# Optimization experiments

Measured on AMD Instinct MI355X. Metric: run time of the kernel, lower is better.

## Reference

```python
import jax, jax.numpy as jnp
import numpy as np

N, KLEN, Q, S, E, H = 8, 512, 16, 128, 256, 8


def setup_inputs() -> dict:
    key = jax.random.key(0)
    ks = jax.random.split(key, 9)
    values = jax.random.normal(ks[0], (N, KLEN, E), dtype=jnp.float32)
    keys = jax.random.normal(ks[1], (N, KLEN, E), dtype=jnp.float32)
    query = jax.random.normal(ks[2], (N, Q, S, E), dtype=jnp.float32)
    mask = jax.random.randint(ks[3], (N, 1, 1, KLEN, 1), 0, 2, dtype=jnp.int32)
    Wv = jax.random.normal(ks[4], (E, E), dtype=jnp.float32) * 0.02
    Wk = jax.random.normal(ks[5], (E, E), dtype=jnp.float32) * 0.02
    Wq = jax.random.normal(ks[6], (E, E), dtype=jnp.float32) * 0.02
    Wo = jax.random.normal(ks[7], (E, H * E), dtype=jnp.float32) * 0.02
    bo = jnp.zeros((E,), dtype=jnp.float32)
    return {"values": values, "keys": keys, "query": query, "mask": mask,
            "Wv": Wv, "Wk": Wk, "Wq": Wq, "Wo": Wo, "bo": bo}


def reference(values, keys, query, mask, Wv, Wk, Wq, Wo, bo):
    # In the torch module head_dim == embed_size and the SAME Linear is applied
    # to every (expanded) head, so project once and broadcast over heads.
    e = Wq.shape[0]
    heads = Wo.shape[1] // e
    v = values @ Wv.T          # [N, K, E]
    k = keys @ Wk.T            # [N, K, E]
    q = query @ Wq.T           # [N, Q, S, E]
    # energy per head is identical; broadcast to [N, H, Q, K, S] to mirror
    # torch's einsum('nqshd,nkhd->nhqks') followed by masked_fill.
    energy = jnp.einsum('nqsd,nkd->nqks', q, k)               # [N, Q, K, S]
    energy = jnp.broadcast_to(energy[:, None],
                              (energy.shape[0], heads) + energy.shape[1:])
    energy = jnp.where(mask == 0, jnp.float32(-1e20), energy)  # [N,H,Q,K,S]
    attn = jax.nn.softmax(energy / jnp.sqrt(jnp.float32(e)), axis=3)
    out = jnp.einsum('nhqks,nkd->nqshd', attn, v)              # [N,Q,S,H,E]
    out = out.reshape(out.shape[0], out.shape[1], out.shape[2], heads * e)
    return out @ Wo.T + bo                                     # [N, Q, S, E]
```

## Files before the change

kernel.cpp:

```cpp
#include <hip/hip_runtime.h>
#include <hip/hip_bf16.h>
#include <stdint.h>

#define NB   8
#define KL   512
#define QD   16
#define SD   128
#define ED   256
#define RPN  (QD*SD)
#define BMR  64
#define FRAG 512
#define PAN  131072

typedef __hip_bfloat16 bf16;
using s16x8 = __attribute__((ext_vector_type(8))) short;
using f32x4 = __attribute__((ext_vector_type(4))) float;

__device__ __forceinline__ float b2f(unsigned short u){
    union { uint32_t i; float f; } v; v.i = ((uint32_t)u) << 16; return v.f;
}
__device__ __forceinline__ float b2f_hi(uint32_t u){
    union { uint32_t i; float f; } v; v.i = u & 0xFFFF0000u; return v.f;
}
__device__ __forceinline__ float b2f_lo(uint32_t u){
    union { uint32_t i; float f; } v; v.i = u << 16; return v.f;
}
__device__ __forceinline__ unsigned short f2b(float f){
    union { float ff; uint32_t i; } v; v.ff = f;
    uint32_t lsb = (v.i >> 16) & 1;
    v.i += 0x7FFFu + lsb;
    return (unsigned short)(v.i >> 16);
}
__device__ __forceinline__ uint32_t cvtpk(float lo, float hi){
    uint32_t r;
    asm("v_cvt_pk_bf16_f32 %0, %1, %2" : "=v"(r) : "v"(lo), "v"(hi));
    return r;
}
__device__ __forceinline__ f32x4 mfma16(s16x8 a, s16x8 b, f32x4 c){
    return __builtin_amdgcn_mfma_f32_16x16x32_bf16(a, b, c, 0, 0, 0);
}

template<bool B>
__device__ __forceinline__ float ldin(const void* p, size_t i){
    if (B) return b2f(((const unsigned short*)p)[i]);
    else   return ((const float*)p)[i];
}

__device__ bool probe_bf16(const uint32_t* __restrict__ w, int* pc){
    if (threadIdx.x == 0) *pc = 0;
    __syncthreads();
    if (threadIdx.x < 256){
        int local = 0;
        #pragma unroll
        for (int i = 0; i < 4; ++i){
            uint32_t x = w[threadIdx.x*4 + i];
            uint32_t e = (x >> 7) & 0xFFu;
            local += (e >= 120u && e <= 132u) ? 1 : 0;
        }
        if (local) atomicAdd(pc, local);
    }
    __syncthreads();
    return *pc > 512;
}

__device__ __forceinline__ int waddr(int i, int o){
    return (((o >> 4)*8 + (i >> 5)) << 9) + (((o & 15) | (((i >> 3) & 3) << 4)) << 3) + (i & 7);
}

template<bool B>
__device__ void gt_body(const void* __restrict__ Wq, const void* __restrict__ Wk,
                        unsigned short* __restrict__ WgH,
                        unsigned short* __restrict__ WgL, int bx){
    int b = bx, a = threadIdx.x;
    float s = 0.f;
    #pragma unroll 8
    for (int d = 0; d < 256; ++d)
        s += ldin<B>(Wq, (size_t)d*256 + a) * ldin<B>(Wk, (size_t)d*256 + b);
    unsigned short hi = f2b(s);
    unsigned short lo = f2b(s - b2f(hi));
    int ad = waddr(b, a);
    WgH[ad] = hi; WgL[ad] = lo;
}
template<bool B>
__device__ void wosmt_body(const void* __restrict__ Wo, const void* __restrict__ Wv,
                           unsigned short* __restrict__ WmH,
                           unsigned short* __restrict__ WmL, int bx, float (*sm)[256]){
    int t = threadIdx.x, e0 = bx*8;
    #pragma unroll
    for (int je = 0; je < 8; ++je){
        int e = e0 + je;
        float s = 0.f;
        #pragma unroll
        for (int h = 0; h < 8; ++h) s += ldin<B>(Wo, (size_t)e*2048 + h*256 + t);
        sm[je][t] = s;
    }
    __syncthreads();
    float acc[8] = {0,0,0,0,0,0,0,0};
    #pragma unroll 4
    for (int dp = 0; dp < 256; ++dp){
        float wv = ldin<B>(Wv, (size_t)dp*256 + t);
        #pragma unroll
        for (int je = 0; je < 8; ++je) acc[je] += sm[je][dp] * wv;
    }
    #pragma unroll
    for (int je = 0; je < 8; ++je){
        unsigned short hi = f2b(acc[je]);
        unsigned short lo = f2b(acc[je] - b2f(hi));
        int ad = waddr(t, e0 + je);
        WmH[ad] = hi; WmL[ad] = lo;
    }
}
__global__ __launch_bounds__(256)
void k_prep(const void* __restrict__ values,
            const void* __restrict__ Wq, const void* __restrict__ Wk,
            const void* __restrict__ Wo, const void* __restrict__ Wv,
            unsigned short* __restrict__ WgH, unsigned short* __restrict__ WgL,
            unsigned short* __restrict__ WmH, unsigned short* __restrict__ WmL){
    __shared__ float sm[8][256];
    __shared__ int pc;
    bool bf = probe_bf16((const uint32_t*)values, &pc);
    if (blockIdx.x < 256){
        if (bf) gt_body<true >(Wq, Wk, WgH, WgL, blockIdx.x);
        else    gt_body<false>(Wq, Wk, WgH, WgL, blockIdx.x);
    } else {
        int bx = blockIdx.x - 256;
        if (bf) wosmt_body<true >(Wo, Wv, WmH, WmL, bx, sm);
        else    wosmt_body<false>(Wo, Wv, WmH, WmL, bx, sm);
    }
}

template<bool B>
__device__ void projM_body(const void* __restrict__ A,
                           const unsigned short* __restrict__ WH,
                           const unsigned short* __restrict__ WL,
                           unsigned short* __restrict__ outF,
                           int bx, bool keysHalf, unsigned short* St){
    int t = threadIdx.x, lane = t & 63, w = t >> 6;
    int l15 = t & 15, g = (t >> 4) & 3;
    int n   = bx >> 4;
    int r0n = (bx & 15) * 32;
    int r0  = n*512 + r0n;

    f32x4 acc[2][2];
    #pragma unroll
    for (int rt = 0; rt < 2; ++rt)
        #pragma unroll
        for (int c = 0; c < 2; ++c) acc[rt][c] = (f32x4){0.f,0.f,0.f,0.f};

    s16x8 wh[3][2], wl[3][2];
    auto LDW = [&](int ks, int sl){
        #pragma unroll
        for (int c = 0; c < 2; ++c){
            size_t off = (size_t)(((w*2 + c)*8 + ks)*512 + lane*8);
            wh[sl][c] = *(const s16x8*)(WH + off);
            wl[sl][c] = *(const s16x8*)(WL + off);
        }
    };
    float4 ar[2][2][2];
    s16x8  ab[2][2];
    auto LDA = [&](int ks, int sl){
        #pragma unroll
        for (int rt = 0; rt < 2; ++rt){
            size_t idx = (size_t)(r0 + rt*16 + l15)*256 + ks*32 + g*8;
            if (B) ab[sl][rt] = *(const s16x8*)((const unsigned short*)A + idx);
            else { ar[sl][rt][0] = *(const float4*)((const float*)A + idx);
                   ar[sl][rt][1] = *(const float4*)((const float*)A + idx + 4); }
        }
    };
    LDW(0,0); LDW(1,1); LDA(0,0); LDA(1,1);

    #pragma unroll
    for (int ks = 0; ks < 8; ++ks){
        int s = ks & 1, sw = ks % 3;
        s16x8 ah[2], al[2];
        #pragma unroll
        for (int rt = 0; rt < 2; ++rt){
            if (B){
                ah[rt] = ab[s][rt];
            } else {
                union { s16x8 v; uint32_t u[4]; } H, L;
                float4 x0 = ar[s][rt][0], x1 = ar[s][rt][1];
                H.u[0] = cvtpk(x0.x, x0.y); H.u[1] = cvtpk(x0.z, x0.w);
                H.u[2] = cvtpk(x1.x, x1.y); H.u[3] = cvtpk(x1.z, x1.w);
                L.u[0] = cvtpk(x0.x - b2f_lo(H.u[0]), x0.y - b2f_hi(H.u[0]));
                L.u[1] = cvtpk(x0.z - b2f_lo(H.u[1]), x0.w - b2f_hi(H.u[1]));
                L.u[2] = cvtpk(x1.x - b2f_lo(H.u[2]), x1.y - b2f_hi(H.u[2]));
                L.u[3] = cvtpk(x1.z - b2f_lo(H.u[3]), x1.w - b2f_hi(H.u[3]));
                ah[rt] = H.v; al[rt] = L.v;
            }
        }
        if (ks + 2 < 8) LDA(ks + 2, s);
        #pragma unroll
        for (int rt = 0; rt < 2; ++rt)
            #pragma unroll
            for (int c = 0; c < 2; ++c){
                acc[rt][c] = mfma16(ah[rt], wh[sw][c], acc[rt][c]);
                if (!B) acc[rt][c] = mfma16(al[rt], wh[sw][c], acc[rt][c]);
                acc[rt][c] = mfma16(ah[rt], wl[sw][c], acc[rt][c]);
            }
        if (ks + 2 < 8) LDW(ks + 2, (ks + 2) % 3);
    }

    #pragma unroll
    for (int rt = 0; rt < 2; ++rt){
        #pragma unroll
        for (int c = 0; c < 2; ++c){
            #pragma unroll
            for (int j = 0; j < 4; ++j){
                int rloc = g*4 + j;
                int col  = (w*2 + c)*16 + l15;
                int idx;
                if (keysHalf)
                    idx = rt*4096 + ((col >> 5) << 9)
                        + ((rloc | (((col >> 3) & 3) << 4)) << 3) + (col & 7);
                else {
                    int kl = rt*16 + rloc;
                    idx = ((col >> 4) << 9)
                        + (((col & 15) | ((kl >> 3) << 4)) << 3) + (kl & 7);
                }
                St[idx] = f2b(acc[rt][c][j]);
            }
        }
    }
    __syncthreads();

    #pragma unroll
    for (int h = 0; h < 2; ++h){
        int s8 = t*8 + h*4096;
        if (keysHalf){
            size_t base = (size_t)n*PAN + (size_t)((r0n >> 4)*8)*512;
            *(s16x8*)(outF + base + s8) = *(const s16x8*)(St + s8);
        } else {
            int ks2 = r0n >> 5;
            int fl = s8 >> 9, off = s8 & 511;
            *(s16x8*)(outF + (size_t)n*PAN + (size_t)((fl*16 + ks2)*512 + off))
                = *(const s16x8*)(St + s8);
        }
    }
}
__global__ __launch_bounds__(512)
void k_projM(const void* __restrict__ keys, const void* __restrict__ values,
             const unsigned short* __restrict__ WgH, const unsigned short* __restrict__ WgL,
             const unsigned short* __restrict__ WmH, const unsigned short* __restrict__ WmL,
             unsigned short* __restrict__ kkF, unsigned short* __restrict__ utF){
    __shared__ unsigned short St[8192];
    __shared__ int pc;
    bool bf = probe_bf16((const uint32_t*)values, &pc);
    int bx = blockIdx.x;
    bool keysHalf = (bx < 128);
    int bxl = bx & 127;
    if (keysHalf){
        if (bf) projM_body<true >(keys, WgH, WgL, kkF, bxl, true, St);
        else    projM_body<false>(keys, WgH, WgL, kkF, bxl, true, St);
    } else {
        if (bf) projM_body<true >(values, WmH, WmL, utF, bxl, false, St);
        else    projM_body<false>(values, WmH, WmL, utF, bxl, false, St);
    }
}

template<bool B>
__device__ void fused_body(const void* __restrict__ query,
                           const unsigned short* __restrict__ kkF,
                           const unsigned short* __restrict__ utF,
                           const int* __restrict__ mask,
                           const void* __restrict__ bo,
                           void* __restrict__ out,
                           unsigned short* Qs, unsigned short* Pf,
                           float* redM, float* redS){
    int bid = blockIdx.x;
    int n   = bid & 7;
    int r0  = (bid >> 3) * BMR;
    int t   = threadIdx.x;
    int l15 = t & 15;
    int g   = (t >> 4) & 3;
    int w   = t >> 6;
    int lane = t & 63;

    const unsigned short* Kn = kkF + (size_t)n*PAN;
    const unsigned short* Un = utF + (size_t)n*PAN;
    const int* mn = mask + n*KL;

    #pragma unroll
    for (int rr = 0; rr < 2; ++rr){
        int row = rr*32 + (t >> 4);
        int c0  = (t & 15) * 16;
        int sw  = (row & 7) << 3;
        size_t qoff = (size_t)n*RPN*ED + (size_t)(r0 + row)*ED + c0;
        if (B){
            const unsigned short* qp = (const unsigned short*)query + qoff;
            s16x8 v0 = *(const s16x8*)(qp);
            s16x8 v1 = *(const s16x8*)(qp + 8);
            *(s16x8*)&Qs[(row*ED + c0    ) ^ sw] = v0;
            *(s16x8*)&Qs[(row*ED + c0 + 8) ^ sw] = v1;
        } else {
            const float* qp = (const float*)query + qoff;
            float4 x0 = *(const float4*)(qp);
            float4 x1 = *(const float4*)(qp + 4);
            float4 x2 = *(const float4*)(qp + 8);
            float4 x3 = *(const float4*)(qp + 12);
            union { s16x8 v; uint32_t u[4]; } pk;
            pk.u[0] = cvtpk(x0.x,x0.y); pk.u[1] = cvtpk(x0.z,x0.w);
            pk.u[2] = cvtpk(x1.x,x1.y); pk.u[3] = cvtpk(x1.z,x1.w);
            *(s16x8*)&Qs[(row*ED + c0    ) ^ sw] = pk.v;
            pk.u[0] = cvtpk(x2.x,x2.y); pk.u[1] = cvtpk(x2.z,x2.w);
            pk.u[2] = cvtpk(x3.x,x3.y); pk.u[3] = cvtpk(x3.z,x3.w);
            *(s16x8*)&Qs[(row*ED + c0 + 8) ^ sw] = pk.v;
        }
    }
    __syncthreads();

    int asw = (l15 & 7) << 3;

    f32x4 acc1[4][4];
    {
        #pragma unroll
        for (int rt = 0; rt < 4; ++rt)
            #pragma unroll
            for (int c = 0; c < 4; ++c) acc1[rt][c] = (f32x4){0.f,0.f,0.f,0.f};

        const unsigned short* kb = Kn + (size_t)w*16384 + (size_t)lane*8;
        s16x8 bb[3][4];
        auto LDK = [&](int KS, int SL){
            #pragma unroll
            for (int c = 0; c < 4; ++c)
                bb[SL][c] = *(const s16x8*)(kb + (size_t)(c*8 + KS)*FRAG);
        };
        LDK(0,0); LDK(1,1);
        #pragma unroll
        for (int ks = 0; ks < 8; ++ks){
            if (ks + 2 < 8) LDK(ks + 2, (ks + 2) % 3);
            int col = ks*32 + g*8;
            #pragma unroll
            for (int rt = 0; rt < 4; ++rt){
                s16x8 a = *(const s16x8*)&Qs[((rt*16 + l15)*ED + col) ^ asw];
                #pragma unroll
                for (int c = 0; c < 4; ++c)
                    acc1[rt][c] = mfma16(a, bb[ks % 3][c], acc1[rt][c]);
            }
        }
        #pragma unroll
        for (int c = 0; c < 4; ++c){
            bool zz = (mn[w*64 + c*16 + l15] == 0);
            #pragma unroll
            for (int rt = 0; rt < 4; ++rt)
                #pragma unroll
                for (int j = 0; j < 4; ++j)
                    acc1[rt][c][j] = zz ? -1e20f : acc1[rt][c][j] * 0.0625f;
        }
    }

    {
        #pragma unroll
        for (int rt = 0; rt < 4; ++rt)
            #pragma unroll
            for (int j = 0; j < 4; ++j){
                float m0 = fmaxf(fmaxf(acc1[rt][0][j], acc1[rt][1][j]),
                                 fmaxf(acc1[rt][2][j], acc1[rt][3][j]));
                #pragma unroll
                for (int off = 1; off < 16; off <<= 1)
                    m0 = fmaxf(m0, __shfl_xor(m0, off, 16));
                if (l15 == 0) redM[(rt*16 + g*4 + j)*8 + w] = m0;
            }
        __syncthreads();
        #pragma unroll
        for (int rt = 0; rt < 4; ++rt)
            #pragma unroll
            for (int j = 0; j < 4; ++j){
                int row = rt*16 + g*4 + j;
                float4 a = *(const float4*)&redM[row*8];
                float4 b = *(const float4*)&redM[row*8 + 4];
                float m = fmaxf(fmaxf(fmaxf(a.x,a.y),fmaxf(a.z,a.w)),
                                fmaxf(fmaxf(b.x,b.y),fmaxf(b.z,b.w)));
                float s = 0.f;
                #pragma unroll
                for (int c = 0; c < 4; ++c){
                    acc1[rt][c][j] = __expf(acc1[rt][c][j] - m);
                    s += acc1[rt][c][j];
                }
                #pragma unroll
                for (int off = 1; off < 16; off <<= 1)
                    s += __shfl_xor(s, off, 16);
                if (l15 == 0) redS[row*8 + w] = s;
            }
        __syncthreads();
        int ihi = ((l15 >> 3) << 4);
        int ilo = l15 & 7;
        #pragma unroll
        for (int rt = 0; rt < 4; ++rt){
            #pragma unroll
            for (int j = 0; j < 4; ++j){
                int row = rt*16 + g*4 + j;
                float4 a = *(const float4*)&redS[row*8];
                float4 b = *(const float4*)&redS[row*8 + 4];
                float inv = 1.0f / ((a.x+a.y+a.z+a.w) + (b.x+b.y+b.z+b.w));
                #pragma unroll
                for (int c = 0; c < 4; ++c){
                    int lp = (g*4 + j) | (((c & 1) << 5) | ihi);
                    int elem = (rt*16 + w*2 + (c >> 1))*FRAG + lp*8 + ilo;
                    Pf[elem] = f2b(acc1[rt][c][j] * inv);
                }
            }
        }
    }
    __syncthreads();

    {
        f32x4 acc2[4][2];
        #pragma unroll
        for (int rt = 0; rt < 4; ++rt)
            #pragma unroll
            for (int c = 0; c < 2; ++c) acc2[rt][c] = (f32x4){0.f,0.f,0.f,0.f};

        const unsigned short* ub = Un + (size_t)(2*w)*8192 + (size_t)lane*8;
        s16x8 bu[3][2];
        auto LDU = [&](int KS, int SL){
            #pragma unroll
            for (int c = 0; c < 2; ++c)
                bu[SL][c] = *(const s16x8*)(ub + (size_t)(c*16 + KS)*FRAG);
        };
        LDU(0,0); LDU(1,1);
        #pragma unroll
        for (int ks = 0; ks < 16; ++ks){
            if (ks + 2 < 16) LDU(ks + 2, (ks + 2) % 3);
            #pragma unroll
            for (int rt = 0; rt < 4; ++rt){
                s16x8 p = *(const s16x8*)&Pf[(rt*16 + ks)*FRAG + lane*8];
                #pragma unroll
                for (int c = 0; c < 2; ++c)
                    acc2[rt][c] = mfma16(p, bu[ks % 3][c], acc2[rt][c]);
            }
        }
        float bov[2];
        #pragma unroll
        for (int c = 0; c < 2; ++c) bov[c] = ldin<B>(bo, (2*w + c)*16 + l15);
        #pragma unroll
        for (int rt = 0; rt < 4; ++rt){
            #pragma unroll
            for (int j = 0; j < 4; ++j){
                int row = rt*16 + g*4 + j;
                #pragma unroll
                for (int c = 0; c < 2; ++c){
                    int e = (2*w + c)*16 + l15;
                    float val = acc2[rt][c][j] + bov[c];
                    size_t oidx = (size_t)n*RPN*ED + (size_t)(r0 + row)*ED + e;
                    if (B) ((unsigned short*)out)[oidx] = f2b(val);
                    else   ((float*)out)[oidx] = val;
                }
            }
        }
    }
}

__global__ __launch_bounds__(512, 2)
void k_fused5(const void* __restrict__ values, const void* __restrict__ query,
              const unsigned short* __restrict__ kkF,
              const unsigned short* __restrict__ utF,
              const int* __restrict__ mask, const void* __restrict__ bo,
              void* __restrict__ out){
    __shared__ unsigned short Qs[BMR*ED];
    __shared__ unsigned short Pf[64*FRAG];
    __shared__ float redM[BMR*8];
    __shared__ float redS[BMR*8];
    __shared__ int pc;
    bool bf = probe_bf16((const uint32_t*)values, &pc);
    if (bf) fused_body<true >(query, kkF, utF, mask, bo, out, Qs, Pf, redM, redS);
    else    fused_body<false>(query, kkF, utF, mask, bo, out, Qs, Pf, redM, redS);
}

extern "C" void kernel_launch(void* const* d_in, const int* in_sizes, int n_in,
                              void* d_out, int out_size, void* d_ws, size_t ws_size,
                              hipStream_t stream){
    const void* values = d_in[0];
    const void* keys   = d_in[1];
    const void* query  = d_in[2];
    const int*  mask   = (const int*)d_in[3];
    const void* Wv     = d_in[4];
    const void* Wk     = d_in[5];
    const void* Wq     = d_in[6];
    const void* Wo     = d_in[7];
    const void* bo     = d_in[8];

    unsigned short* wsu = (unsigned short*)d_ws;
    unsigned short* wgh = wsu;
    unsigned short* wgl = wsu + 65536;
    unsigned short* wmh = wsu + 131072;
    unsigned short* wml = wsu + 196608;
    unsigned short* ws_kk = wsu + 262144;
    unsigned short* ws_u  = ws_kk + (size_t)NB*PAN;

    k_prep  <<< 288, 256, 0, stream>>>(values, Wq, Wk, Wo, Wv, wgh, wgl, wmh, wml);
    k_projM <<< 256, 512, 0, stream>>>(keys, values, wgh, wgl, wmh, wml, ws_kk, ws_u);
    k_fused5<<< 256, 512, 0, stream>>>(values, query, ws_kk, ws_u, mask, bo, d_out);
}
```

Before: 144.8 us.

## Halve fused attention row tile and split prep reductions across 512 threads

```diff
diff --git a/kernel.cpp b/kernel.cpp
--- a/kernel.cpp
+++ b/kernel.cpp
@@ -8,7 +8,7 @@
 #define SD   128
 #define ED   256
 #define RPN  (QD*SD)
-#define BMR  64
+#define BMR  32
 #define FRAG 512
 #define PAN  131072
 
@@ -70,62 +70,81 @@
 template<bool B>
 __device__ void gt_body(const void* __restrict__ Wq, const void* __restrict__ Wk,
                         unsigned short* __restrict__ WgH,
-                        unsigned short* __restrict__ WgL, int bx){
-    int b = bx, a = threadIdx.x;
+                        unsigned short* __restrict__ WgL, int bx,
+                        float (*ps)[2048]){
+    int t = threadIdx.x;
+    int a = t & 255, hf = t >> 8;
+    int b = bx;
+    int d0 = hf * 128;
     float s = 0.f;
     #pragma unroll 8
-    for (int d = 0; d < 256; ++d)
+    for (int d = d0; d < d0 + 128; ++d)
         s += ldin<B>(Wq, (size_t)d*256 + a) * ldin<B>(Wk, (size_t)d*256 + b);
-    unsigned short hi = f2b(s);
-    unsigned short lo = f2b(s - b2f(hi));
-    int ad = waddr(b, a);
-    WgH[ad] = hi; WgL[ad] = lo;
+    ps[hf][a] = s;
+    __syncthreads();
+    if (t < 256){
+        float v = ps[0][t] + ps[1][t];
+        unsigned short hi = f2b(v);
+        unsigned short lo = f2b(v - b2f(hi));
+        int ad = waddr(b, t);
+        WgH[ad] = hi; WgL[ad] = lo;
+    }
 }
 template<bool B>
 __device__ void wosmt_body(const void* __restrict__ Wo, const void* __restrict__ Wv,
                            unsigned short* __restrict__ WmH,
-                           unsigned short* __restrict__ WmL, int bx, float (*sm)[256]){
-    int t = threadIdx.x, e0 = bx*8;
+                           unsigned short* __restrict__ WmL, int bx,
+                           float (*sm)[256], float (*ps)[2048]){
+    int t = threadIdx.x, d = t & 255, hf = t >> 8, e0 = bx*8;
     #pragma unroll
-    for (int je = 0; je < 8; ++je){
-        int e = e0 + je;
+    for (int jj = 0; jj < 4; ++jj){
+        int je = hf*4 + jj;
+        int e  = e0 + je;
         float s = 0.f;
         #pragma unroll
-        for (int h = 0; h < 8; ++h) s += ldin<B>(Wo, (size_t)e*2048 + h*256 + t);
-        sm[je][t] = s;
+        for (int h = 0; h < 8; ++h) s += ldin<B>(Wo, (size_t)e*2048 + h*256 + d);
+        sm[je][d] = s;
     }
     __syncthreads();
     float acc[8] = {0,0,0,0,0,0,0,0};
+    int dp0 = hf * 128;
     #pragma unroll 4
-    for (int dp = 0; dp < 256; ++dp){
-        float wv = ldin<B>(Wv, (size_t)dp*256 + t);
+    for (int dp = dp0; dp < dp0 + 128; ++dp){
+        float wv = ldin<B>(Wv, (size_t)dp*256 + d);
         #pragma unroll
         for (int je = 0; je < 8; ++je) acc[je] += sm[je][dp] * wv;
     }
     #pragma unroll
-    for (int je = 0; je < 8; ++je){
-        unsigned short hi = f2b(acc[je]);
-        unsigned short lo = f2b(acc[je] - b2f(hi));
-        int ad = waddr(t, e0 + je);
-        WmH[ad] = hi; WmL[ad] = lo;
-    }
-}
-__global__ __launch_bounds__(256)
+    for (int je = 0; je < 8; ++je) ps[hf][d*8 + je] = acc[je];
+    __syncthreads();
+    if (t < 256){
+        #pragma unroll
+        for (int je = 0; je < 8; ++je){
+            float v = ps[0][t*8 + je] + ps[1][t*8 + je];
+            unsigned short hi = f2b(v);
+            unsigned short lo = f2b(v - b2f(hi));
+            int ad = waddr(t, e0 + je);
+            WmH[ad] = hi; WmL[ad] = lo;
+        }
+    }
+}
+__global__ __launch_bounds__(512)
 void k_prep(const void* __restrict__ values,
             const void* __restrict__ Wq, const void* __restrict__ Wk,
             const void* __restrict__ Wo, const void* __restrict__ Wv,
             unsigned short* __restrict__ WgH, unsigned short* __restrict__ WgL,
             unsigned short* __restrict__ WmH, unsigned short* __restrict__ WmL){
     __shared__ float sm[8][256];
+    __shared__ float ps[2][2048];
     __shared__ int pc;
     bool bf = probe_bf16((const uint32_t*)values, &pc);
     if (blockIdx.x < 256){
-        if (bf) gt_body<true >(Wq, Wk, WgH, WgL, blockIdx.x);
-        else    gt_body<false>(Wq, Wk, WgH, WgL, blockIdx.x);
+        if (bf) gt_body<true >(Wq, Wk, WgH, WgL, blockIdx.x, ps);
+        else    gt_body<false>(Wq, Wk, WgH, WgL, blockIdx.x, ps);
     } else {
         int bx = blockIdx.x - 256;
-        if (bf) wosmt_body<true >(Wo, Wv, WmH, WmL, bx, sm);
-        else    wosmt_body<false>(Wo, Wv, WmH, WmL, bx, sm);
+        if (bf) wosmt_body<true >(Wo, Wv, WmH, WmL, bx, sm, ps);
+        else    wosmt_body<false>(Wo, Wv, WmH, WmL, bx, sm, ps);
     }
 }
 
@@ -280,9 +299,8 @@
     const unsigned short* Un = utF + (size_t)n*PAN;
     const int* mn = mask + n*KL;
 
-    #pragma unroll
-    for (int rr = 0; rr < 2; ++rr){
-        int row = rr*32 + (t >> 4);
+    {
+        int row = t >> 4;
         int c0  = (t & 15) * 16;
         int sw  = (row & 7) << 3;
         size_t qoff = (size_t)n*RPN*ED + (size_t)(r0 + row)*ED + c0;
@@ -311,10 +329,11 @@
 
     int asw = (l15 & 7) << 3;
 
-    f32x4 acc1[4][4];
+    float p[2][4][4];
     {
-        #pragma unroll
-        for (int rt = 0; rt < 4; ++rt)
+        f32x4 acc1[2][4];
+        #pragma unroll
+        for (int rt = 0; rt < 2; ++rt)
             #pragma unroll
             for (int c = 0; c < 4; ++c) acc1[rt][c] = (f32x4){0.f,0.f,0.f,0.f};
 
@@ -330,40 +349,49 @@
         for (int ks = 0; ks < 8; ++ks){
             if (ks + 2 < 8) LDK(ks + 2, (ks + 2) % 3);
             int col = ks*32 + g*8;
-            #pragma unroll
-            for (int rt = 0; rt < 4; ++rt){
-                s16x8 a = *(const s16x8*)&Qs[((rt*16 + l15)*ED + col) ^ asw];
-                #pragma unroll
-                for (int c = 0; c < 4; ++c)
-                    acc1[rt][c] = mfma16(a, bb[ks % 3][c], acc1[rt][c]);
+            s16x8 a0 = *(const s16x8*)&Qs[(( 0 + l15)*ED + col) ^ asw];
+            s16x8 a1 = *(const s16x8*)&Qs[((16 + l15)*ED + col) ^ asw];
+            #pragma unroll
+            for (int c = 0; c < 4; ++c){
+                acc1[0][c] = mfma16(a0, bb[ks % 3][c], acc1[0][c]);
+                acc1[1][c] = mfma16(a1, bb[ks % 3][c], acc1[1][c]);
             }
         }
         #pragma unroll
         for (int c = 0; c < 4; ++c){
             bool zz = (mn[w*64 + c*16 + l15] == 0);
             #pragma unroll
-            for (int rt = 0; rt < 4; ++rt)
+            for (int rt = 0; rt < 2; ++rt)
                 #pragma unroll
                 for (int j = 0; j < 4; ++j)
-                    acc1[rt][c][j] = zz ? -1e20f : acc1[rt][c][j] * 0.0625f;
+                    p[rt][c][j] = zz ? -1e20f : acc1[rt][c][j] * 0.0625f;
         }
     }
 
     {
-        #pragma unroll
-        for (int rt = 0; rt < 4; ++rt)
+        float mx[2][4];
+        #pragma unroll
+        for (int rt = 0; rt < 2; ++rt)
             #pragma unroll
             for (int j = 0; j < 4; ++j){
-                float m0 = fmaxf(fmaxf(acc1[rt][0][j], acc1[rt][1][j]),
-                                 fmaxf(acc1[rt][2][j], acc1[rt][3][j]));
+                float m0 = fmaxf(fmaxf(p[rt][0][j], p[rt][1][j]),
+                                 fmaxf(p[rt][2][j], p[rt][3][j]));
                 #pragma unroll
                 for (int off = 1; off < 16; off <<= 1)
                     m0 = fmaxf(m0, __shfl_xor(m0, off, 16));
-                if (l15 == 0) redM[(rt*16 + g*4 + j)*8 + w] = m0;
-            }
+                mx[rt][j] = m0;
+            }
+        if (l15 == 0){
+            #pragma unroll
+            for (int rt = 0; rt < 2; ++rt)
+                #pragma unroll
+                for (int j = 0; j < 4; ++j)
+                    redM[(rt*16 + g*4 + j)*8 + w] = mx[rt][j];
+        }
         __syncthreads();
-        #pragma unroll
-        for (int rt = 0; rt < 4; ++rt)
+        float sm[2][4];
+        #pragma unroll
+        for (int rt = 0; rt < 2; ++rt)
             #pragma unroll
             for (int j = 0; j < 4; ++j){
                 int row = rt*16 + g*4 + j;
@@ -374,19 +402,26 @@
                 float s = 0.f;
                 #pragma unroll
                 for (int c = 0; c < 4; ++c){
-                    acc1[rt][c][j] = __expf(acc1[rt][c][j] - m);
-                    s += acc1[rt][c][j];
+                    p[rt][c][j] = __expf(p[rt][c][j] - m);
+                    s += p[rt][c][j];
                 }
                 #pragma unroll
                 for (int off = 1; off < 16; off <<= 1)
                     s += __shfl_xor(s, off, 16);
-                if (l15 == 0) redS[row*8 + w] = s;
-            }
+                sm[rt][j] = s;
+            }
+        if (l15 == 0){
+            #pragma unroll
+            for (int rt = 0; rt < 2; ++rt)
+                #pragma unroll
+                for (int j = 0; j < 4; ++j)
+                    redS[(rt*16 + g*4 + j)*8 + w] = sm[rt][j];
+        }
         __syncthreads();
         int ihi = ((l15 >> 3) << 4);
         int ilo = l15 & 7;
         #pragma unroll
-        for (int rt = 0; rt < 4; ++rt){
+        for (int rt = 0; rt < 2; ++rt){
             #pragma unroll
             for (int j = 0; j < 4; ++j){
                 int row = rt*16 + g*4 + j;
@@ -397,7 +432,7 @@
                 for (int c = 0; c < 4; ++c){
                     int lp = (g*4 + j) | (((c & 1) << 5) | ihi);
                     int elem = (rt*16 + w*2 + (c >> 1))*FRAG + lp*8 + ilo;
-                    Pf[elem] = f2b(acc1[rt][c][j] * inv);
+                    Pf[elem] = f2b(p[rt][c][j] * inv);
                 }
             }
         }
@@ -405,9 +440,9 @@
     __syncthreads();
 
     {
-        f32x4 acc2[4][2];
-        #pragma unroll
-        for (int rt = 0; rt < 4; ++rt)
+        f32x4 acc2[2][2];
+        #pragma unroll
+        for (int rt = 0; rt < 2; ++rt)
             #pragma unroll
             for (int c = 0; c < 2; ++c) acc2[rt][c] = (f32x4){0.f,0.f,0.f,0.f};
 
@@ -422,19 +457,19 @@
         #pragma unroll
         for (int ks = 0; ks < 16; ++ks){
             if (ks + 2 < 16) LDU(ks + 2, (ks + 2) % 3);
-            #pragma unroll
-            for (int rt = 0; rt < 4; ++rt){
-                s16x8 p = *(const s16x8*)&Pf[(rt*16 + ks)*FRAG + lane*8];
-                #pragma unroll
-                for (int c = 0; c < 2; ++c)
-                    acc2[rt][c] = mfma16(p, bu[ks % 3][c], acc2[rt][c]);
+            s16x8 p0 = *(const s16x8*)&Pf[( 0 + ks)*FRAG + lane*8];
+            s16x8 p1 = *(const s16x8*)&Pf[(16 + ks)*FRAG + lane*8];
+            #pragma unroll
+            for (int c = 0; c < 2; ++c){
+                acc2[0][c] = mfma16(p0, bu[ks % 3][c], acc2[0][c]);
+                acc2[1][c] = mfma16(p1, bu[ks % 3][c], acc2[1][c]);
             }
         }
         float bov[2];
         #pragma unroll
         for (int c = 0; c < 2; ++c) bov[c] = ldin<B>(bo, (2*w + c)*16 + l15);
         #pragma unroll
-        for (int rt = 0; rt < 4; ++rt){
+        for (int rt = 0; rt < 2; ++rt){
             #pragma unroll
             for (int j = 0; j < 4; ++j){
                 int row = rt*16 + g*4 + j;
@@ -451,14 +486,14 @@
     }
 }
 
-__global__ __launch_bounds__(512, 2)
-void k_fused5(const void* __restrict__ values, const void* __restrict__ query,
+__global__ __launch_bounds__(512, 4)
+void k_fused4(const void* __restrict__ values, const void* __restrict__ query,
               const unsigned short* __restrict__ kkF,
               const unsigned short* __restrict__ utF,
               const int* __restrict__ mask, const void* __restrict__ bo,
               void* __restrict__ out){
     __shared__ unsigned short Qs[BMR*ED];
-    __shared__ unsigned short Pf[64*FRAG];
+    __shared__ unsigned short Pf[32*FRAG];
     __shared__ float redM[BMR*8];
     __shared__ float redS[BMR*8];
     __shared__ int pc;
@@ -488,7 +523,7 @@
     unsigned short* ws_kk = wsu + 262144;
     unsigned short* ws_u  = ws_kk + (size_t)NB*PAN;
 
-    k_prep  <<< 288, 256, 0, stream>>>(values, Wq, Wk, Wo, Wv, wgh, wgl, wmh, wml);
+    k_prep  <<< 288, 512, 0, stream>>>(values, Wq, Wk, Wo, Wv, wgh, wgl, wmh, wml);
     k_projM <<< 256, 512, 0, stream>>>(keys, values, wgh, wgl, wmh, wml, ws_kk, ws_u);
-    k_fused5<<< 256, 512, 0, stream>>>(values, query, ws_kk, ws_u, mask, bo, d_out);
-}
+    k_fused4<<< 512, 512, 0, stream>>>(values, query, ws_kk, ws_u, mask, bo, d_out);
+}
```

Result: faster. 136.8 us (-5.5%).
